# Optimization experiments

Measured on AMD Instinct MI355X. Metric: run time of the kernel, lower is better.

## Reference

```python
import jax, jax.numpy as jnp
import numpy as np

NUM_BINS = 15
NUM_CLASSES = 4
NEIGHBORHOOD_WIDTH = 3  # K; num_neighbor_classes = K**2 = 9


def _neighbor_counts(onehot):
    """Count of same-class neighbors in KxK window (center excluded), zero padding.
    onehot: [B, C, H, W] float32 one-hot of hard predictions.
    returns int32 [B, C, H, W] in [0, K^2-1].
    """
    K = NEIGHBORHOOD_WIDTH
    C = onehot.shape[1]
    kern = np.ones((K, K), dtype=np.float32)
    kern[K // 2, K // 2] = 0.0  # exclude center pixel
    kernel = jnp.asarray(np.broadcast_to(kern, (C, 1, K, K)).copy())  # depthwise OIHW
    counts = jax.lax.conv_general_dilated(
        onehot, kernel,
        window_strides=(1, 1), padding='SAME',
        feature_group_count=C,
        dimension_numbers=('NCHW', 'OIHW', 'NCHW'))
    return jnp.clip(jnp.round(counts).astype(jnp.int32), 0, K * K - 1)


def setup_inputs() -> dict:
    key = jax.random.key(0)
    k1, k2 = jax.random.split(key)
    logits = jax.random.normal(k1, (16, NUM_CLASSES, 512, 512), dtype=jnp.float32)
    # calibration frequency table: val_freqs[class][neighbor_count][conf_bin]
    val_freqs = jax.random.uniform(k2, (NUM_CLASSES, NEIGHBORHOOD_WIDTH ** 2, NUM_BINS), dtype=jnp.float32)
    return {"logits": logits, "val_freqs": val_freqs}


def reference(logits, val_freqs):
    B, C, H, W = logits.shape
    probs = jax.nn.softmax(logits, axis=1)                      # [B,C,H,W]
    y_hard = jnp.argmax(probs, axis=1)                          # [B,H,W]

    # (y_hard == lab_idx) for every class at once -> one-hot [B,C,H,W]
    onehot = jax.nn.one_hot(y_hard, C, axis=1, dtype=jnp.float32)
    agg = _neighbor_counts(onehot)                              # [B,C,H,W] int32 in [0, K^2-1]

    # confidence bin per pixel/class: uniform bins on [0,1]
    bin_width = 1.0 / NUM_BINS
    bin_map = jnp.clip((probs / bin_width).astype(jnp.int32), 0, NUM_BINS - 1)  # [B,C,H,W]

    # fused multi-index gather replacing the nested class/neighbor-mask loops:
    # calibrated[b,c,h,w] = val_freqs[c, agg[b,c,h,w], bin_map[b,c,h,w]]
    cls_idx = jnp.arange(C, dtype=jnp.int32)[None, :, None, None]
    calibrated = val_freqs[cls_idx, agg, bin_map]               # [B,C,H,W]

    # normalize across classes, guarding zero sums
    s = jnp.sum(calibrated, axis=1, keepdims=True)
    s = jnp.where(s == 0, 1.0, s)
    return calibrated / s
```

## Files before the change

### kernel.cpp

```cpp
#include <hip/hip_runtime.h>

#define HW (512 * 512)

__global__ __launch_bounds__(256) void nectar_binning_kernel(
    const float* __restrict__ logits,
    const float* __restrict__ val_freqs,
    float* __restrict__ out)
{
    constexpr int TX = 32, TY = 8;
    __shared__ int cls[(TY + 2) * (TX + 2)];
    __shared__ float vf[540];

    const int b  = blockIdx.z;
    const int w0 = blockIdx.x * TX;
    const int h0 = blockIdx.y * TY;
    const int tid = threadIdx.y * TX + threadIdx.x;

    for (int i = tid; i < 540; i += 256) vf[i] = val_freqs[i];

    const float* lb = logits + (size_t)b * 4 * HW;

    for (int i = tid; i < (TY + 2) * (TX + 2); i += 256) {
        int ly = i / (TX + 2);
        int lx = i - ly * (TX + 2);
        int h = h0 + ly - 1;
        int w = w0 + lx - 1;
        int c = 4;
        if ((unsigned)h < 512u && (unsigned)w < 512u) {
            int base = (h << 9) + w;
            float x0 = lb[base];
            float x1 = lb[HW + base];
            float x2 = lb[2 * HW + base];
            float x3 = lb[3 * HW + base];
            float best = x0; c = 0;
            if (x1 > best) { best = x1; c = 1; }
            if (x2 > best) { best = x2; c = 2; }
            if (x3 > best) { best = x3; c = 3; }
        }
        cls[i] = c;
    }
    __syncthreads();

    const int lx = threadIdx.x, ly = threadIdx.y;
    const int h = h0 + ly, w = w0 + lx;
    const int base = (h << 9) + w;

    float x0 = lb[base];
    float x1 = lb[HW + base];
    float x2 = lb[2 * HW + base];
    float x3 = lb[3 * HW + base];
    float m = fmaxf(fmaxf(x0, x1), fmaxf(x2, x3));
    float e0 = expf(x0 - m), e1 = expf(x1 - m);
    float e2 = expf(x2 - m), e3 = expf(x3 - m);
    float s = ((e0 + e1) + e2) + e3;
    float p[4];
    p[0] = e0 / s; p[1] = e1 / s; p[2] = e2 / s; p[3] = e3 / s;

    unsigned long long packed = 0;
    #pragma unroll
    for (int dy = 0; dy < 3; dy++) {
        #pragma unroll
        for (int dx = 0; dx < 3; dx++) {
            if (dy == 1 && dx == 1) continue;
            packed += 1ull << (cls[(ly + dy) * (TX + 2) + (lx + dx)] * 8);
        }
    }

    constexpr float bw = 1.0f / 15.0f;
    float cal[4];
    float cs = 0.0f;
    #pragma unroll
    for (int c = 0; c < 4; c++) {
        int cnt = (int)((packed >> (8 * c)) & 0xFFull);
        int bin = (int)(p[c] / bw);
        bin = bin > 14 ? 14 : bin;
        float v = vf[c * 135 + cnt * 15 + bin];
        cal[c] = v;
        cs += v;
    }
    if (cs == 0.0f) cs = 1.0f;
    float inv = 1.0f / cs;

    float* ob = out + (size_t)b * 4 * HW + base;
    #pragma unroll
    for (int c = 0; c < 4; c++) ob[c * HW] = cal[c] * inv;
}

extern "C" void kernel_launch(void* const* d_in, const int* in_sizes, int n_in,
                              void* d_out, int out_size, void* d_ws, size_t ws_size,
                              hipStream_t stream) {
    const float* logits    = (const float*)d_in[0];
    const float* val_freqs = (const float*)d_in[1];
    float* out             = (float*)d_out;

    dim3 block(32, 8, 1);
    dim3 grid(512 / 32, 512 / 8, 16);
    hipLaunchKernelGGL(nectar_binning_kernel, grid, block, 0, stream,
                       logits, val_freqs, out);
}
```

Baseline: 136.0 us.

## Process 2x2 pixels per thread with packed nibble neighbor counts and float2 I/O

Each thread now handles a 2x2 pixel quad in a 64x16 tile, which shrinks the halo overhead per block. Logits are read and outputs written with float2 vector accesses. Neighbor counts are packed as 4-bit nibbles in 32-bit words and built from shared column sums across the quad. The softmax divide uses a fast reciprocal, with an exact-divide fallback when a value lands near a bin boundary, and the final normalization uses rcp. The risks are higher register pressure, a divergent fallback branch, and approximate-reciprocal differences in the output.

Measured after the change: 129.7 us. -4.7%, faster.

```diff
diff --git a/kernel.cpp b/kernel.cpp
--- a/kernel.cpp
+++ b/kernel.cpp
@@ -1,89 +1,139 @@
 #include <hip/hip_runtime.h>
 
 #define HW (512 * 512)
+
+constexpr int TX = 64, TY = 16;
+constexpr int CW = TX + 2;
+constexpr int CH = TY + 2;
+constexpr float BWIDTH = 1.0f / 15.0f;
+constexpr float DELTA = 2e-5f;
 
 __global__ __launch_bounds__(256) void nectar_binning_kernel(
     const float* __restrict__ logits,
     const float* __restrict__ val_freqs,
     float* __restrict__ out)
 {
-    constexpr int TX = 32, TY = 8;
-    __shared__ int cls[(TY + 2) * (TX + 2)];
+    __shared__ unsigned int cls[CH * CW];
     __shared__ float vf[540];
 
     const int b  = blockIdx.z;
     const int w0 = blockIdx.x * TX;
     const int h0 = blockIdx.y * TY;
-    const int tid = threadIdx.y * TX + threadIdx.x;
+    const int tid = threadIdx.y * 32 + threadIdx.x;
 
     for (int i = tid; i < 540; i += 256) vf[i] = val_freqs[i];
 
     const float* lb = logits + (size_t)b * 4 * HW;
 
-    for (int i = tid; i < (TY + 2) * (TX + 2); i += 256) {
-        int ly = i / (TX + 2);
-        int lx = i - ly * (TX + 2);
-        int h = h0 + ly - 1;
-        int w = w0 + lx - 1;
-        int c = 4;
-        if ((unsigned)h < 512u && (unsigned)w < 512u) {
-            int base = (h << 9) + w;
+    for (int i = tid; i < CH * CW; i += 256) {
+        int ly = i / CW;
+        int lx = i - ly * CW;
+        int hh = h0 + ly - 1;
+        int ww = w0 + lx - 1;
+        unsigned int v = 0;
+        if ((unsigned)hh < 512u && (unsigned)ww < 512u) {
+            int base = (hh << 9) + ww;
             float x0 = lb[base];
             float x1 = lb[HW + base];
             float x2 = lb[2 * HW + base];
             float x3 = lb[3 * HW + base];
-            float best = x0; c = 0;
+            int c = 0; float best = x0;
             if (x1 > best) { best = x1; c = 1; }
             if (x2 > best) { best = x2; c = 2; }
             if (x3 > best) { best = x3; c = 3; }
+            v = 1u << (4 * c);
         }
-        cls[i] = c;
+        cls[i] = v;
     }
     __syncthreads();
 
-    const int lx = threadIdx.x, ly = threadIdx.y;
-    const int h = h0 + ly, w = w0 + lx;
-    const int base = (h << 9) + w;
+    const int tx = threadIdx.x;
+    const int ty = threadIdx.y;
+    const int w  = w0 + 2 * tx;
+    const int h  = h0 + 2 * ty;
 
-    float x0 = lb[base];
-    float x1 = lb[HW + base];
-    float x2 = lb[2 * HW + base];
-    float x3 = lb[3 * HW + base];
-    float m = fmaxf(fmaxf(x0, x1), fmaxf(x2, x3));
-    float e0 = expf(x0 - m), e1 = expf(x1 - m);
-    float e2 = expf(x2 - m), e3 = expf(x3 - m);
-    float s = ((e0 + e1) + e2) + e3;
-    float p[4];
-    p[0] = e0 / s; p[1] = e1 / s; p[2] = e2 / s; p[3] = e3 / s;
-
-    unsigned long long packed = 0;
+    float x[2][4][2];
     #pragma unroll
-    for (int dy = 0; dy < 3; dy++) {
+    for (int jy = 0; jy < 2; jy++) {
+        int base = ((h + jy) << 9) + w;
         #pragma unroll
-        for (int dx = 0; dx < 3; dx++) {
-            if (dy == 1 && dx == 1) continue;
-            packed += 1ull << (cls[(ly + dy) * (TX + 2) + (lx + dx)] * 8);
+        for (int c = 0; c < 4; c++) {
+            float2 v = *reinterpret_cast<const float2*>(lb + (size_t)c * HW + base);
+            x[jy][c][0] = v.x; x[jy][c][1] = v.y;
         }
     }
 
-    constexpr float bw = 1.0f / 15.0f;
-    float cal[4];
-    float cs = 0.0f;
+    unsigned int rowv[4][4];
     #pragma unroll
-    for (int c = 0; c < 4; c++) {
-        int cnt = (int)((packed >> (8 * c)) & 0xFFull);
-        int bin = (int)(p[c] / bw);
-        bin = bin > 14 ? 14 : bin;
-        float v = vf[c * 135 + cnt * 15 + bin];
-        cal[c] = v;
-        cs += v;
+    for (int r = 0; r < 4; r++) {
+        const unsigned int* rp = &cls[(2 * ty + r) * CW + 2 * tx];
+        rowv[r][0] = rp[0]; rowv[r][1] = rp[1]; rowv[r][2] = rp[2]; rowv[r][3] = rp[3];
     }
-    if (cs == 0.0f) cs = 1.0f;
-    float inv = 1.0f / cs;
+    unsigned int coltop[4], colbot[4];
+    #pragma unroll
+    for (int j = 0; j < 4; j++) {
+        unsigned int mid = rowv[1][j] + rowv[2][j];
+        coltop[j] = mid + rowv[0][j];
+        colbot[j] = mid + rowv[3][j];
+    }
+    unsigned int packed[2][2];
+    packed[0][0] = coltop[0] + coltop[1] + coltop[2] - rowv[1][1];
+    packed[0][1] = coltop[1] + coltop[2] + coltop[3] - rowv[1][2];
+    packed[1][0] = colbot[0] + colbot[1] + colbot[2] - rowv[2][1];
+    packed[1][1] = colbot[1] + colbot[2] + colbot[3] - rowv[2][2];
 
-    float* ob = out + (size_t)b * 4 * HW + base;
+    float* ob = out + (size_t)b * 4 * HW;
+
     #pragma unroll
-    for (int c = 0; c < 4; c++) ob[c * HW] = cal[c] * inv;
+    for (int jy = 0; jy < 2; jy++) {
+        float res[2][4];
+        #pragma unroll
+        for (int jx = 0; jx < 2; jx++) {
+            float x0 = x[jy][0][jx], x1 = x[jy][1][jx], x2 = x[jy][2][jx], x3 = x[jy][3][jx];
+            float m = fmaxf(fmaxf(x0, x1), fmaxf(x2, x3));
+            float e[4];
+            e[0] = expf(x0 - m); e[1] = expf(x1 - m);
+            e[2] = expf(x2 - m); e[3] = expf(x3 - m);
+            float s = ((e[0] + e[1]) + e[2]) + e[3];
+
+            float rs = __builtin_amdgcn_rcpf(s);
+            float q[4];
+            bool slow = false;
+            #pragma unroll
+            for (int c = 0; c < 4; c++) {
+                q[c] = (e[c] * rs) * 15.0f;
+                float f = q[c] - floorf(q[c]);
+                slow |= (f < DELTA) | (f > 1.0f - DELTA);
+            }
+            if (slow) {
+                #pragma unroll
+                for (int c = 0; c < 4; c++) q[c] = (e[c] / s) / BWIDTH;
+            }
+
+            unsigned int pk = packed[jy][jx];
+            float cs = 0.0f;
+            float cal[4];
+            #pragma unroll
+            for (int c = 0; c < 4; c++) {
+                int bin = (int)q[c];
+                bin = bin > 14 ? 14 : bin;
+                int cnt = (int)((pk >> (4 * c)) & 0xFu);
+                float v = vf[c * 135 + cnt * 15 + bin];
+                cal[c] = v;
+                cs += v;
+            }
+            if (cs == 0.0f) cs = 1.0f;
+            float inv = __builtin_amdgcn_rcpf(cs);
+            #pragma unroll
+            for (int c = 0; c < 4; c++) res[jx][c] = cal[c] * inv;
+        }
+        int base = ((h + jy) << 9) + w;
+        #pragma unroll
+        for (int c = 0; c < 4; c++) {
+            float2 v; v.x = res[0][c]; v.y = res[1][c];
+            *reinterpret_cast<float2*>(ob + (size_t)c * HW + base) = v;
+        }
+    }
 }
 
 extern "C" void kernel_launch(void* const* d_in, const int* in_sizes, int n_in,
@@ -94,7 +144,7 @@
     float* out             = (float*)d_out;
 
     dim3 block(32, 8, 1);
-    dim3 grid(512 / 32, 512 / 8, 16);
+    dim3 grid(512 / TX, 512 / TY, 16);
     hipLaunchKernelGGL(nectar_binning_kernel, grid, block, 0, stream,
                        logits, val_freqs, out);
 }
```
